# Kernel optimization log

Measured on AMD Instinct MI355X. Metric: run time of the kernel, lower is better.

The kernel has to match this reference:

```python
import jax, jax.numpy as jnp
import numpy as np

# Correlation hyperparameters (from init_kwargs):
PAD = 4            # pad_size
KERNEL = 1         # kernel_size (point-wise)
MD = 4             # max_displacement
STRIDE1 = 1
STRIDE2 = 1

B, C, H, W = 8, 256, 96, 160


def setup_inputs() -> dict:
    key = jax.random.key(0)
    k1, k2 = jax.random.split(key)
    input1 = jax.random.normal(k1, (B, C, H, W), dtype=jnp.float32)
    input2 = jax.random.normal(k2, (B, C, H, W), dtype=jnp.float32)
    return {"input1": input1, "input2": input2}


def reference(input1, input2):
    """FlowNet-style correlation cost volume.

    out[b, (dy+MD)*D + (dx+MD), y, x] = (1/C) * sum_c in1[b,c,y,x] * in2pad[b,c,y+dy+PAD, x+dx+PAD]
    where in2pad is input2 zero-padded by PAD and D = 2*MD+1. With PAD == MD,
    kernel_size == 1, stride1 == stride2 == 1 the output is [B, D*D, H, W].
    """
    b, c, h, w = input1.shape
    in2p = jnp.pad(input2, ((0, 0), (0, 0), (PAD, PAD), (PAD, PAD)))
    D = 2 * MD + 1
    outs = []
    # Fixed small 81-iteration loop over displacements (not a data dim).
    for dy in range(0, 2 * MD + 1, STRIDE2):
        for dx in range(0, 2 * MD + 1, STRIDE2):
            shifted = jax.lax.dynamic_slice(in2p, (0, 0, dy, dx), (b, c, h, w))
            # mean over channels == sum / (kernel^2 * C) with kernel == 1
            outs.append(jnp.mean(input1 * shifted, axis=1))
    return jnp.stack(outs, axis=1)  # [B, 81, H, W]
```

## Files before the change

kernel.cpp:

```cpp
#include <hip/hip_runtime.h>
#include <stdint.h>

#define B_ 8
#define C_ 256
#define H_ 96
#define W_ 160
#define ND 9
#define NDISP 81
#define NCHUNK 128
#define TX 8
#define NXG 20
#define NTHR 256
#define NCOMP 180
#define IN2_OFF 640
#define ROW_B 688
#define BUF_B 6912
#define NBUF 4
#define NSEG 418
#define HW (H_ * W_)
#define CHSTEP (2 * HW)

typedef __attribute__((ext_vector_type(2))) _Float16 half2v;

__device__ __forceinline__ unsigned pk(float lo, float hi) {
    return __builtin_bit_cast(unsigned, __builtin_amdgcn_cvt_pkrtz(lo, hi));
}
__device__ __forceinline__ float dot2acc(unsigned a, unsigned w, float acc) {
#if __has_builtin(__builtin_amdgcn_fdot2)
    return __builtin_amdgcn_fdot2(__builtin_bit_cast(half2v, a),
                                  __builtin_bit_cast(half2v, w), acc, false);
#else
    half2v av = __builtin_bit_cast(half2v, a);
    half2v wv = __builtin_bit_cast(half2v, w);
    return acc + (float)av.x * (float)wv.x + (float)av.y * (float)wv.y;
#endif
}

__device__ __forceinline__ const float* seg_src(int s, int b, int y,
        const float* in1, const float* in2, int* woff)
{
    if (s < 40) {
        *woff = s * 16;
        return in1 + ((size_t)(b * C_) * H_ + y) * W_ + 4 * s;
    }
    const int t = s - 40;
    const int r = t / 42, k = t - r * 42;
    *woff = IN2_OFF + r * ROW_B + k * 16;
    int row = y + r - 4;
    row = row < 0 ? 0 : (row >= H_ ? H_ - 1 : row);
    int x = 4 * k - 4;
    x = x < 0 ? 0 : (x > W_ - 4 ? W_ - 4 : x);
    return in2 + ((size_t)(b * C_) * H_ + row) * W_ + x;
}

__global__ __launch_bounds__(NTHR) void corr_alldy_kernel(
    const float* __restrict__ in1,
    const float* __restrict__ in2,
    float* __restrict__ out)
{
    __shared__ __align__(16) unsigned lds[NBUF * BUF_B / 4];

    const int tid = threadIdx.x;
    const int b   = blockIdx.x & 7;
    const int y   = blockIdx.x >> 3;

    int w0off, w1off = 0;
    const float* p0 = seg_src(tid, b, y, in1, in2, &w0off);
    const bool v1 = (tid + NTHR) < NSEG;
    const float* p1 = in1;
    if (v1) p1 = seg_src(tid + NTHR, b, y, in1, in2, &w1off);

    const bool isComp = (tid < NCOMP);
    const int  dy = isComp ? (tid / NXG) : 0;
    const int  xg = isComp ? (tid % NXG) : 0;
    const int  x0 = TX * xg;
    const bool rowOk = (y + dy - 4 >= 0) && (y + dy - 4 < H_);
    const bool mzW0 = (xg == 0);
    const bool mzW3 = (xg == NXG - 1);

    const int aof = 32 * xg;
    const int wof = IN2_OFF + dy * ROW_B + 32 * xg;

    float acc[ND][TX];
    #pragma unroll
    for (int dx = 0; dx < ND; ++dx)
        #pragma unroll
        for (int j = 0; j < TX; ++j) acc[dx][j] = 0.f;

    float4 SAp0, SAp1, SAq0, SAq1;
    float4 SBp0, SBp1, SBq0, SBq1;

    #define LOADS(S) do {                                                     \
        S##p0 = *(const float4*)(p0);  S##p1 = *(const float4*)(p0 + HW);     \
        S##q0 = *(const float4*)(p1);  S##q1 = *(const float4*)(p1 + HW);     \
        p0 += CHSTEP; p1 += CHSTEP;                                           \
    } while (0);

    #define CVTW(BUFI, S) do {                                                \
        char* base = (char*)lds + (BUFI) * BUF_B;                             \
        *(uint4*)(base + w0off) = make_uint4(                                 \
            pk(S##p0.x, S##p1.x), pk(S##p0.y, S##p1.y),                       \
            pk(S##p0.z, S##p1.z), pk(S##p0.w, S##p1.w));                      \
        if (v1) *(uint4*)(base + w1off) = make_uint4(                         \
            pk(S##q0.x, S##q1.x), pk(S##q0.y, S##q1.y),                       \
            pk(S##q0.z, S##q1.z), pk(S##q0.w, S##q1.w));                      \
    } while (0);

    #define COMPUTE(BUFI)                                                     \
    if (isComp) {                                                             \
        const char* bb = (const char*)lds + (BUFI) * BUF_B;                   \
        uint4 A0 = *(const uint4*)(bb + aof);                                 \
        uint4 A1 = *(const uint4*)(bb + aof + 16);                            \
        uint4 W0 = *(const uint4*)(bb + wof);                                 \
        uint4 W1 = *(const uint4*)(bb + wof + 16);                            \
        uint4 W2 = *(const uint4*)(bb + wof + 32);                            \
        uint4 W3 = *(const uint4*)(bb + wof + 48);                            \
        if (mzW0) W0 = make_uint4(0u, 0u, 0u, 0u);                            \
        if (mzW3) W3 = make_uint4(0u, 0u, 0u, 0u);                            \
        unsigned a[8]  = {A0.x, A0.y, A0.z, A0.w, A1.x, A1.y, A1.z, A1.w};    \
        unsigned w[16] = {W0.x, W0.y, W0.z, W0.w, W1.x, W1.y, W1.z, W1.w,     \
                          W2.x, W2.y, W2.z, W2.w, W3.x, W3.y, W3.z, W3.w};    \
        _Pragma("unroll")                                                     \
        for (int dx = 0; dx < ND; ++dx) {                                     \
            _Pragma("unroll")                                                 \
            for (int j = 0; j < TX; ++j)                                      \
                acc[dx][j] = dot2acc(a[j], w[dx + j], acc[dx][j]);            \
        }                                                                     \
    }

    #define BODY(KM4, SWR, SLD, DOW, DOL)                                     \
        if (DOW) { CVTW(((KM4) + 2) & 3, SWR) }                               \
        if (DOL) { LOADS(SLD) }                                               \
        COMPUTE(KM4)                                                          \
        __syncthreads();

    LOADS(SA)
    CVTW(0, SA)
    LOADS(SA)
    CVTW(1, SA)
    LOADS(SB)
    __syncthreads();

    #pragma unroll 1
    for (int g = 0; g < 31; ++g) {
        BODY(0, SB, SA, true, true)
        BODY(1, SA, SB, true, true)
        BODY(2, SB, SA, true, true)
        BODY(3, SA, SB, true, true)
    }
    BODY(0, SB, SA, true, true)
    BODY(1, SA, SB, true, false)
    BODY(2, SA, SA, false, false)
    BODY(3, SA, SA, false, false)

    #undef BODY
    #undef COMPUTE
    #undef CVTW
    #undef LOADS

    if (isComp) {
        const float m = rowOk ? (1.0f / (float)C_) : 0.f;
        float* outp = out + ((size_t)(b * NDISP + dy * ND) * H_ + y) * W_ + x0;
        #pragma unroll
        for (int dx = 0; dx < ND; ++dx) {
            float4 o0 = make_float4(acc[dx][0] * m, acc[dx][1] * m,
                                    acc[dx][2] * m, acc[dx][3] * m);
            float4 o1 = make_float4(acc[dx][4] * m, acc[dx][5] * m,
                                    acc[dx][6] * m, acc[dx][7] * m);
            *(float4*)(outp + dx * HW)     = o0;
            *(float4*)(outp + dx * HW + 4) = o1;
        }
    }
}

extern "C" void kernel_launch(void* const* d_in, const int* in_sizes, int n_in,
                              void* d_out, int out_size, void* d_ws, size_t ws_size,
                              hipStream_t stream) {
    const float* in1 = (const float*)d_in[0];
    const float* in2 = (const float*)d_in[1];
    float* out = (float*)d_out;

    const int grid = B_ * H_;
    corr_alldy_kernel<<<grid, NTHR, 0, stream>>>(in1, in2, out);
}
```

Measured before the change: 110.3 us.

## Split each output row into two half-width blocks with 4-pixel thread tiles

Each block now handles half of an output row (80 pixels) instead of the full row, and the grid doubles to 1536 blocks. Each thread computes a 4-wide x tile instead of 8, so the accumulator array, LDS buffers and per-block global loads shrink. The aim is more blocks and waves in flight and lower register pressure, giving better occupancy and latency hiding. The cost is more redundant halo loads of in2 and fewer dot products per LDS read.

```diff
diff --git a/kernel.cpp b/kernel.cpp
--- a/kernel.cpp
+++ b/kernel.cpp
@@ -8,15 +8,15 @@
 #define ND 9
 #define NDISP 81
 #define NCHUNK 128
-#define TX 8
+#define TX 4
 #define NXG 20
 #define NTHR 256
 #define NCOMP 180
-#define IN2_OFF 640
-#define ROW_B 688
-#define BUF_B 6912
+#define IN2_OFF 320
+#define ROW_B 352
+#define BUF_B 3584
 #define NBUF 4
-#define NSEG 418
+#define NSEG 218
 #define HW (H_ * W_)
 #define CHSTEP (2 * HW)
 
@@ -36,24 +36,24 @@
 #endif
 }
 
-__device__ __forceinline__ const float* seg_src(int s, int b, int y,
+__device__ __forceinline__ const float* seg_src(int s, int b, int y, int h,
         const float* in1, const float* in2, int* woff)
 {
-    if (s < 40) {
+    if (s < 20) {
         *woff = s * 16;
-        return in1 + ((size_t)(b * C_) * H_ + y) * W_ + 4 * s;
+        return in1 + ((size_t)(b * C_) * H_ + y) * W_ + 80 * h + 4 * s;
     }
-    const int t = s - 40;
-    const int r = t / 42, k = t - r * 42;
+    const int t = s - 20;
+    const int r = t / 22, k = t - r * 22;
     *woff = IN2_OFF + r * ROW_B + k * 16;
     int row = y + r - 4;
     row = row < 0 ? 0 : (row >= H_ ? H_ - 1 : row);
-    int x = 4 * k - 4;
+    int x = 80 * h - 4 + 4 * k;
     x = x < 0 ? 0 : (x > W_ - 4 ? W_ - 4 : x);
     return in2 + ((size_t)(b * C_) * H_ + row) * W_ + x;
 }
 
-__global__ __launch_bounds__(NTHR) void corr_alldy_kernel(
+__global__ __launch_bounds__(NTHR) void corr_hx16_kernel(
     const float* __restrict__ in1,
     const float* __restrict__ in2,
     float* __restrict__ out)
@@ -62,24 +62,25 @@
 
     const int tid = threadIdx.x;
     const int b   = blockIdx.x & 7;
-    const int y   = blockIdx.x >> 3;
+    const int idx = blockIdx.x >> 3;
+    const int y   = idx >> 1;
+    const int h   = idx & 1;
 
-    int w0off, w1off = 0;
-    const float* p0 = seg_src(tid, b, y, in1, in2, &w0off);
-    const bool v1 = (tid + NTHR) < NSEG;
-    const float* p1 = in1;
-    if (v1) p1 = seg_src(tid + NTHR, b, y, in1, in2, &w1off);
+    int w0off = 0;
+    const bool v0 = tid < NSEG;
+    const float* p0 = in1;
+    if (v0) p0 = seg_src(tid, b, y, h, in1, in2, &w0off);
 
     const bool isComp = (tid < NCOMP);
     const int  dy = isComp ? (tid / NXG) : 0;
     const int  xg = isComp ? (tid % NXG) : 0;
-    const int  x0 = TX * xg;
+    const int  x0 = 80 * h + TX * xg;
     const bool rowOk = (y + dy - 4 >= 0) && (y + dy - 4 < H_);
-    const bool mzW0 = (xg == 0);
-    const bool mzW3 = (xg == NXG - 1);
+    const bool mzW0 = (h == 0) && (xg == 0);
+    const bool mzW2 = (h == 1) && (xg == NXG - 1);
 
-    const int aof = 32 * xg;
-    const int wof = IN2_OFF + dy * ROW_B + 32 * xg;
+    const int aof = 16 * xg;
+    const int wof = IN2_OFF + dy * ROW_B + 16 * xg;
 
     float acc[ND][TX];
     #pragma unroll
@@ -87,39 +88,35 @@
         #pragma unroll
         for (int j = 0; j < TX; ++j) acc[dx][j] = 0.f;
 
-    float4 SAp0, SAp1, SAq0, SAq1;
-    float4 SBp0, SBp1, SBq0, SBq1;
+    float4 SAp0, SAp1;
+    float4 SBp0, SBp1;
 
     #define LOADS(S) do {                                                     \
         S##p0 = *(const float4*)(p0);  S##p1 = *(const float4*)(p0 + HW);     \
-        S##q0 = *(const float4*)(p1);  S##q1 = *(const float4*)(p1 + HW);     \
-        p0 += CHSTEP; p1 += CHSTEP;                                           \
+        p0 += CHSTEP;                                                         \
     } while (0);
 
     #define CVTW(BUFI, S) do {                                                \
-        char* base = (char*)lds + (BUFI) * BUF_B;                             \
-        *(uint4*)(base + w0off) = make_uint4(                                 \
-            pk(S##p0.x, S##p1.x), pk(S##p0.y, S##p1.y),                       \
-            pk(S##p0.z, S##p1.z), pk(S##p0.w, S##p1.w));                      \
-        if (v1) *(uint4*)(base + w1off) = make_uint4(                         \
-            pk(S##q0.x, S##q1.x), pk(S##q0.y, S##q1.y),                       \
-            pk(S##q0.z, S##q1.z), pk(S##q0.w, S##q1.w));                      \
+        if (v0) {                                                             \
+            char* base = (char*)lds + (BUFI) * BUF_B;                         \
+            *(uint4*)(base + w0off) = make_uint4(                             \
+                pk(S##p0.x, S##p1.x), pk(S##p0.y, S##p1.y),                   \
+                pk(S##p0.z, S##p1.z), pk(S##p0.w, S##p1.w));                  \
+        }                                                                     \
     } while (0);
 
     #define COMPUTE(BUFI)                                                     \
     if (isComp) {                                                             \
         const char* bb = (const char*)lds + (BUFI) * BUF_B;                   \
         uint4 A0 = *(const uint4*)(bb + aof);                                 \
-        uint4 A1 = *(const uint4*)(bb + aof + 16);                            \
         uint4 W0 = *(const uint4*)(bb + wof);                                 \
         uint4 W1 = *(const uint4*)(bb + wof + 16);                            \
         uint4 W2 = *(const uint4*)(bb + wof + 32);                            \
-        uint4 W3 = *(const uint4*)(bb + wof + 48);                            \
         if (mzW0) W0 = make_uint4(0u, 0u, 0u, 0u);                            \
-        if (mzW3) W3 = make_uint4(0u, 0u, 0u, 0u);                            \
-        unsigned a[8]  = {A0.x, A0.y, A0.z, A0.w, A1.x, A1.y, A1.z, A1.w};    \
-        unsigned w[16] = {W0.x, W0.y, W0.z, W0.w, W1.x, W1.y, W1.z, W1.w,     \
-                          W2.x, W2.y, W2.z, W2.w, W3.x, W3.y, W3.z, W3.w};    \
+        if (mzW2) W2 = make_uint4(0u, 0u, 0u, 0u);                            \
+        unsigned a[4]  = {A0.x, A0.y, A0.z, A0.w};                            \
+        unsigned w[12] = {W0.x, W0.y, W0.z, W0.w, W1.x, W1.y, W1.z, W1.w,     \
+                          W2.x, W2.y, W2.z, W2.w};                            \
         _Pragma("unroll")                                                     \
         for (int dx = 0; dx < ND; ++dx) {                                     \
             _Pragma("unroll")                                                 \
@@ -163,12 +160,9 @@
         float* outp = out + ((size_t)(b * NDISP + dy * ND) * H_ + y) * W_ + x0;
         #pragma unroll
         for (int dx = 0; dx < ND; ++dx) {
-            float4 o0 = make_float4(acc[dx][0] * m, acc[dx][1] * m,
-                                    acc[dx][2] * m, acc[dx][3] * m);
-            float4 o1 = make_float4(acc[dx][4] * m, acc[dx][5] * m,
-                                    acc[dx][6] * m, acc[dx][7] * m);
-            *(float4*)(outp + dx * HW)     = o0;
-            *(float4*)(outp + dx * HW + 4) = o1;
+            float4 o = make_float4(acc[dx][0] * m, acc[dx][1] * m,
+                                   acc[dx][2] * m, acc[dx][3] * m);
+            *(float4*)(outp + dx * HW) = o;
         }
     }
 }
@@ -180,6 +174,6 @@
     const float* in2 = (const float*)d_in[1];
     float* out = (float*)d_out;
 
-    const int grid = B_ * H_;
-    corr_alldy_kernel<<<grid, NTHR, 0, stream>>>(in1, in2, out);
+    const int grid = B_ * H_ * 2;
+    corr_hx16_kernel<<<grid, NTHR, 0, stream>>>(in1, in2, out);
 }
```

Measured after the change: 111.1 us (median of 2 runs). About the same (+0.8%).

## Split block into dedicated producer and consumer wavefronts

Applied to the files above, without the earlier changes.

Warp-specializes the block. Threads 192-255 (one wavefront) now do all global loads and fp16 packing into LDS, each covering up to 7 segments. Threads 0-179 only compute the dot products from LDS, so load and compute latency can overlap across wavefronts instead of every thread doing both. The cost is a single producer wave that must issue all loads. That concentrates the memory traffic and register pressure in one wave and may make it the bottleneck.

```diff
diff --git a/kernel.cpp b/kernel.cpp
--- a/kernel.cpp
+++ b/kernel.cpp
@@ -12,6 +12,7 @@
 #define NXG 20
 #define NTHR 256
 #define NCOMP 180
+#define PBASE 192
 #define IN2_OFF 640
 #define ROW_B 688
 #define BUF_B 6912
@@ -53,7 +54,7 @@
     return in2 + ((size_t)(b * C_) * H_ + row) * W_ + x;
 }
 
-__global__ __launch_bounds__(NTHR) void corr_alldy_kernel(
+__global__ __launch_bounds__(NTHR) void corr_pc_kernel(
     const float* __restrict__ in1,
     const float* __restrict__ in2,
     float* __restrict__ out)
@@ -63,12 +64,22 @@
     const int tid = threadIdx.x;
     const int b   = blockIdx.x & 7;
     const int y   = blockIdx.x >> 3;
-
-    int w0off, w1off = 0;
-    const float* p0 = seg_src(tid, b, y, in1, in2, &w0off);
-    const bool v1 = (tid + NTHR) < NSEG;
-    const float* p1 = in1;
-    if (v1) p1 = seg_src(tid + NTHR, b, y, in1, in2, &w1off);
+    const bool isProd = (tid >= PBASE);
+    const int  pl = tid - PBASE;
+
+    int of0=0, of1=0, of2=0, of3=0, of4=0, of5=0, of6=0;
+    const float *q0=in1, *q1=in1, *q2=in1, *q3=in1, *q4=in1, *q5=in1, *q6=in1;
+    bool v6 = false;
+    if (isProd) {
+        q0 = seg_src(pl,        b, y, in1, in2, &of0);
+        q1 = seg_src(pl + 64,   b, y, in1, in2, &of1);
+        q2 = seg_src(pl + 128,  b, y, in1, in2, &of2);
+        q3 = seg_src(pl + 192,  b, y, in1, in2, &of3);
+        q4 = seg_src(pl + 256,  b, y, in1, in2, &of4);
+        q5 = seg_src(pl + 320,  b, y, in1, in2, &of5);
+        v6 = (pl + 384) < NSEG;
+        if (v6) q6 = seg_src(pl + 384, b, y, in1, in2, &of6);
+    }
 
     const bool isComp = (tid < NCOMP);
     const int  dy = isComp ? (tid / NXG) : 0;
@@ -77,9 +88,8 @@
     const bool rowOk = (y + dy - 4 >= 0) && (y + dy - 4 < H_);
     const bool mzW0 = (xg == 0);
     const bool mzW3 = (xg == NXG - 1);
-
-    const int aof = 32 * xg;
-    const int wof = IN2_OFF + dy * ROW_B + 32 * xg;
+    const int  aof = 32 * xg;
+    const int  wof = IN2_OFF + dy * ROW_B + 32 * xg;
 
     float acc[ND][TX];
     #pragma unroll
@@ -87,23 +97,33 @@
         #pragma unroll
         for (int j = 0; j < TX; ++j) acc[dx][j] = 0.f;
 
-    float4 SAp0, SAp1, SAq0, SAq1;
-    float4 SBp0, SBp1, SBq0, SBq1;
-
-    #define LOADS(S) do {                                                     \
-        S##p0 = *(const float4*)(p0);  S##p1 = *(const float4*)(p0 + HW);     \
-        S##q0 = *(const float4*)(p1);  S##q1 = *(const float4*)(p1 + HW);     \
-        p0 += CHSTEP; p1 += CHSTEP;                                           \
+    float4 La0, La1, Lb0, Lb1, Lc0, Lc1, Ld0, Ld1, Le0, Le1, Lf0, Lf1, Lg0, Lg1;
+
+    #define LOADS do {                                                        \
+        La0 = *(const float4*)(q0); La1 = *(const float4*)(q0 + HW);          \
+        Lb0 = *(const float4*)(q1); Lb1 = *(const float4*)(q1 + HW);          \
+        Lc0 = *(const float4*)(q2); Lc1 = *(const float4*)(q2 + HW);          \
+        Ld0 = *(const float4*)(q3); Ld1 = *(const float4*)(q3 + HW);          \
+        Le0 = *(const float4*)(q4); Le1 = *(const float4*)(q4 + HW);          \
+        Lf0 = *(const float4*)(q5); Lf1 = *(const float4*)(q5 + HW);          \
+        Lg0 = *(const float4*)(q6); Lg1 = *(const float4*)(q6 + HW);          \
+        q0 += CHSTEP; q1 += CHSTEP; q2 += CHSTEP; q3 += CHSTEP;               \
+        q4 += CHSTEP; q5 += CHSTEP; q6 += CHSTEP;                             \
     } while (0);
 
-    #define CVTW(BUFI, S) do {                                                \
+    #define PKW(base, off, R0, R1)                                            \
+        *(uint4*)((base) + (off)) = make_uint4(                               \
+            pk(R0.x, R1.x), pk(R0.y, R1.y), pk(R0.z, R1.z), pk(R0.w, R1.w));
+
+    #define CVTW(BUFI) do {                                                   \
         char* base = (char*)lds + (BUFI) * BUF_B;                             \
-        *(uint4*)(base + w0off) = make_uint4(                                 \
-            pk(S##p0.x, S##p1.x), pk(S##p0.y, S##p1.y),                       \
-            pk(S##p0.z, S##p1.z), pk(S##p0.w, S##p1.w));                      \
-        if (v1) *(uint4*)(base + w1off) = make_uint4(                         \
-            pk(S##q0.x, S##q1.x), pk(S##q0.y, S##q1.y),                       \
-            pk(S##q0.z, S##q1.z), pk(S##q0.w, S##q1.w));                      \
+        PKW(base, of0, La0, La1)                                              \
+        PKW(base, of1, Lb0, Lb1)                                              \
+        PKW(base, of2, Lc0, Lc1)                                              \
+        PKW(base, of3, Ld0, Ld1)                                              \
+        PKW(base, of4, Le0, Le1)                                              \
+        PKW(base, of5, Lf0, Lf1)                                              \
+        if (v6) { PKW(base, of6, Lg0, Lg1) }                                  \
     } while (0);
 
     #define COMPUTE(BUFI)                                                     \
@@ -128,34 +148,38 @@
         }                                                                     \
     }
 
-    #define BODY(KM4, SWR, SLD, DOW, DOL)                                     \
-        if (DOW) { CVTW(((KM4) + 2) & 3, SWR) }                               \
-        if (DOL) { LOADS(SLD) }                                               \
-        COMPUTE(KM4)                                                          \
+    #define BODY(KM4, DOW, DOL)                                               \
+        if (isProd) {                                                         \
+            if (DOW) { CVTW(((KM4) + 2) & 3) }                                \
+            if (DOL) { LOADS }                                                \
+        } else { COMPUTE(KM4) }                                               \
         __syncthreads();
 
-    LOADS(SA)
-    CVTW(0, SA)
-    LOADS(SA)
-    CVTW(1, SA)
-    LOADS(SB)
+    if (isProd) {
+        LOADS
+        CVTW(0)
+        LOADS
+        CVTW(1)
+        LOADS
+    }
     __syncthreads();
 
     #pragma unroll 1
     for (int g = 0; g < 31; ++g) {
-        BODY(0, SB, SA, true, true)
-        BODY(1, SA, SB, true, true)
-        BODY(2, SB, SA, true, true)
-        BODY(3, SA, SB, true, true)
-    }
-    BODY(0, SB, SA, true, true)
-    BODY(1, SA, SB, true, false)
-    BODY(2, SA, SA, false, false)
-    BODY(3, SA, SA, false, false)
+        BODY(0, true, true)
+        BODY(1, true, true)
+        BODY(2, true, true)
+        BODY(3, true, true)
+    }
+    BODY(0, true, true)
+    BODY(1, true, false)
+    BODY(2, false, false)
+    BODY(3, false, false)
 
     #undef BODY
     #undef COMPUTE
     #undef CVTW
+    #undef PKW
     #undef LOADS
 
     if (isComp) {
@@ -181,5 +205,5 @@
     float* out = (float*)d_out;
 
     const int grid = B_ * H_;
-    corr_alldy_kernel<<<grid, NTHR, 0, stream>>>(in1, in2, out);
-}
+    corr_pc_kernel<<<grid, NTHR, 0, stream>>>(in1, in2, out);
+}
```

New measurement: 188.5 us. +70.9%, slower.

## Split rows into quarter-width single-wave blocks without barriers

Applied to the files above, without the earlier changes.

Each block now covers a quarter of an image row with one 64-thread wavefront, instead of a full row with 256 threads. The grid grows fourfold, and the LDS staging drops from four buffers to two. Because each block is a single wave, all __syncthreads calls are removed and the software pipeline becomes a plain double-buffered compute/convert/load sequence. The goal is to remove barrier stalls and raise occupancy through smaller blocks. The costs are extra halo loads of input2 for each quarter, and reliance on in-wave ordering of LDS accesses with no explicit barrier.

```diff
diff --git a/kernel.cpp b/kernel.cpp
--- a/kernel.cpp
+++ b/kernel.cpp
@@ -9,14 +9,13 @@
 #define NDISP 81
 #define NCHUNK 128
 #define TX 8
-#define NXG 20
-#define NTHR 256
-#define NCOMP 180
-#define IN2_OFF 640
-#define ROW_B 688
-#define BUF_B 6912
-#define NBUF 4
-#define NSEG 418
+#define NXG 5
+#define NTHR 64
+#define NCOMP 45
+#define IN2_OFF 160
+#define ROW_B 192
+#define BUF_B 1888
+#define NSEG 118
 #define HW (H_ * W_)
 #define CHSTEP (2 * HW)
 
@@ -30,53 +29,56 @@
     return __builtin_amdgcn_fdot2(__builtin_bit_cast(half2v, a),
                                   __builtin_bit_cast(half2v, w), acc, false);
 #else
-    half2v av = __builtin_bit_cast(half2v, a);
-    half2v wv = __builtin_bit_cast(half2v, w);
-    return acc + (float)av.x * (float)wv.x + (float)av.y * (float)wv.y;
+    float r;
+    asm("v_dot2_f32_f16 %0, %1, %2, %3"
+        : "=v"(r) : "v"(a), "v"(w), "v"(acc));
+    return r;
 #endif
 }
 
-__device__ __forceinline__ const float* seg_src(int s, int b, int y,
+__device__ __forceinline__ const float* seg_src(int s, int b, int y, int q,
         const float* in1, const float* in2, int* woff)
 {
-    if (s < 40) {
+    if (s < 10) {
         *woff = s * 16;
-        return in1 + ((size_t)(b * C_) * H_ + y) * W_ + 4 * s;
+        return in1 + ((size_t)(b * C_) * H_ + y) * W_ + 40 * q + 4 * s;
     }
-    const int t = s - 40;
-    const int r = t / 42, k = t - r * 42;
+    const int t = s - 10;
+    const int r = t / 12, k = t - r * 12;
     *woff = IN2_OFF + r * ROW_B + k * 16;
     int row = y + r - 4;
     row = row < 0 ? 0 : (row >= H_ ? H_ - 1 : row);
-    int x = 4 * k - 4;
+    int x = 40 * q - 4 + 4 * k;
     x = x < 0 ? 0 : (x > W_ - 4 ? W_ - 4 : x);
     return in2 + ((size_t)(b * C_) * H_ + row) * W_ + x;
 }
 
-__global__ __launch_bounds__(NTHR) void corr_alldy_kernel(
+__global__ __launch_bounds__(NTHR) void corr_q1w_kernel(
     const float* __restrict__ in1,
     const float* __restrict__ in2,
     float* __restrict__ out)
 {
-    __shared__ __align__(16) unsigned lds[NBUF * BUF_B / 4];
+    __shared__ __align__(16) unsigned lds[2 * BUF_B / 4];
 
-    const int tid = threadIdx.x;
-    const int b   = blockIdx.x & 7;
-    const int y   = blockIdx.x >> 3;
+    const int tid  = threadIdx.x;
+    const int b    = blockIdx.x & 7;
+    const int rest = blockIdx.x >> 3;
+    const int y    = rest >> 2;
+    const int q    = rest & 3;
 
-    int w0off, w1off = 0;
-    const float* p0 = seg_src(tid, b, y, in1, in2, &w0off);
-    const bool v1 = (tid + NTHR) < NSEG;
+    int w0off = 0, w1off = 0;
+    const float* p0 = seg_src(tid, b, y, q, in1, in2, &w0off);
+    const bool v1 = (tid + 64) < NSEG;
     const float* p1 = in1;
-    if (v1) p1 = seg_src(tid + NTHR, b, y, in1, in2, &w1off);
+    if (v1) p1 = seg_src(tid + 64, b, y, q, in1, in2, &w1off);
 
     const bool isComp = (tid < NCOMP);
     const int  dy = isComp ? (tid / NXG) : 0;
     const int  xg = isComp ? (tid % NXG) : 0;
-    const int  x0 = TX * xg;
+    const int  x0 = 40 * q + TX * xg;
     const bool rowOk = (y + dy - 4 >= 0) && (y + dy - 4 < H_);
-    const bool mzW0 = (xg == 0);
-    const bool mzW3 = (xg == NXG - 1);
+    const bool mzW0 = (q == 0) && (xg == 0);
+    const bool mzW3 = (q == 3) && (xg == NXG - 1);
 
     const int aof = 32 * xg;
     const int wof = IN2_OFF + dy * ROW_B + 32 * xg;
@@ -87,27 +89,25 @@
         #pragma unroll
         for (int j = 0; j < TX; ++j) acc[dx][j] = 0.f;
 
-    float4 SAp0, SAp1, SAq0, SAq1;
-    float4 SBp0, SBp1, SBq0, SBq1;
+    float4 Sp0, Sp1, Sq0, Sq1;
 
-    #define LOADS(S) do {                                                     \
-        S##p0 = *(const float4*)(p0);  S##p1 = *(const float4*)(p0 + HW);     \
-        S##q0 = *(const float4*)(p1);  S##q1 = *(const float4*)(p1 + HW);     \
+    #define LOADS do {                                                        \
+        Sp0 = *(const float4*)(p0);  Sp1 = *(const float4*)(p0 + HW);         \
+        Sq0 = *(const float4*)(p1);  Sq1 = *(const float4*)(p1 + HW);         \
         p0 += CHSTEP; p1 += CHSTEP;                                           \
     } while (0);
 
-    #define CVTW(BUFI, S) do {                                                \
+    #define CVTW(BUFI) do {                                                   \
         char* base = (char*)lds + (BUFI) * BUF_B;                             \
         *(uint4*)(base + w0off) = make_uint4(                                 \
-            pk(S##p0.x, S##p1.x), pk(S##p0.y, S##p1.y),                       \
-            pk(S##p0.z, S##p1.z), pk(S##p0.w, S##p1.w));                      \
+            pk(Sp0.x, Sp1.x), pk(Sp0.y, Sp1.y),                               \
+            pk(Sp0.z, Sp1.z), pk(Sp0.w, Sp1.w));                              \
         if (v1) *(uint4*)(base + w1off) = make_uint4(                         \
-            pk(S##q0.x, S##q1.x), pk(S##q0.y, S##q1.y),                       \
-            pk(S##q0.z, S##q1.z), pk(S##q0.w, S##q1.w));                      \
+            pk(Sq0.x, Sq1.x), pk(Sq0.y, Sq1.y),                               \
+            pk(Sq0.z, Sq1.z), pk(Sq0.w, Sq1.w));                              \
     } while (0);
 
-    #define COMPUTE(BUFI)                                                     \
-    if (isComp) {                                                             \
+    #define COMPUTE(BUFI) {                                                   \
         const char* bb = (const char*)lds + (BUFI) * BUF_B;                   \
         uint4 A0 = *(const uint4*)(bb + aof);                                 \
         uint4 A1 = *(const uint4*)(bb + aof + 16);                            \
@@ -128,30 +128,22 @@
         }                                                                     \
     }
 
-    #define BODY(KM4, SWR, SLD, DOW, DOL)                                     \
-        if (DOW) { CVTW(((KM4) + 2) & 3, SWR) }                               \
-        if (DOL) { LOADS(SLD) }                                               \
-        COMPUTE(KM4)                                                          \
-        __syncthreads();
+    #define BODY(BUFI, DOW, DOL)                                              \
+        COMPUTE(BUFI)                                                         \
+        if (DOW) { CVTW((BUFI) ^ 1) }                                         \
+        if (DOL) { LOADS }
 
-    LOADS(SA)
-    CVTW(0, SA)
-    LOADS(SA)
-    CVTW(1, SA)
-    LOADS(SB)
-    __syncthreads();
+    LOADS
+    CVTW(0)
+    LOADS
 
     #pragma unroll 1
-    for (int g = 0; g < 31; ++g) {
-        BODY(0, SB, SA, true, true)
-        BODY(1, SA, SB, true, true)
-        BODY(2, SB, SA, true, true)
-        BODY(3, SA, SB, true, true)
+    for (int g = 0; g < 63; ++g) {
+        BODY(0, true, true)
+        BODY(1, true, true)
     }
-    BODY(0, SB, SA, true, true)
-    BODY(1, SA, SB, true, false)
-    BODY(2, SA, SA, false, false)
-    BODY(3, SA, SA, false, false)
+    BODY(0, true, false)
+    BODY(1, false, false)
 
     #undef BODY
     #undef COMPUTE
@@ -180,6 +172,6 @@
     const float* in2 = (const float*)d_in[1];
     float* out = (float*)d_out;
 
-    const int grid = B_ * H_;
-    corr_alldy_kernel<<<grid, NTHR, 0, stream>>>(in1, in2, out);
+    const int grid = B_ * H_ * 4;
+    corr_q1w_kernel<<<grid, NTHR, 0, stream>>>(in1, in2, out);
 }
```

After: 207.3 us. 1.88x slower.
